# Performance work log

Measured on AMD Instinct MI355X. Metric: run time of the kernel, lower is better.

The kernel has to match this reference:

```python
import jax, jax.numpy as jnp
import numpy as np

B, T, A, OBS = 4096, 32, 4, 115
H, K, ACT = 64, 8, 19
FEAT = 4 + 3 + 4 * A          # 23 structured features
IN_DIM = FEAT + ACT * A       # 99 with action one-hots


def setup_inputs() -> dict:
    key = jax.random.key(0)
    ks = jax.random.split(key, 16)
    s = lambda *sh: 1.0 / np.sqrt(sh[-1])
    inp = {
        "obs_seq": jax.random.normal(ks[0], (B, T, A, OBS), jnp.float32),
        "action_seq": jax.random.randint(ks[1], (B, T, A), 0, ACT, jnp.int32),
        # feature_proj: Linear(IN_DIM->H) + LayerNorm(H)
        "proj_W": jax.random.normal(ks[2], (H, IN_DIM), jnp.float32) * s(H, IN_DIM),
        "proj_b": jnp.zeros((H,), jnp.float32),
        "ln_g": jnp.ones((H,), jnp.float32),
        "ln_b": jnp.zeros((H,), jnp.float32),
        # 2-layer GRU
        "Wih0": jax.random.normal(ks[3], (3 * H, H), jnp.float32) * s(1, H),
        "Whh0": jax.random.normal(ks[4], (3 * H, H), jnp.float32) * s(1, H),
        "bih0": jnp.zeros((3 * H,), jnp.float32),
        "bhh0": jnp.zeros((3 * H,), jnp.float32),
        "Wih1": jax.random.normal(ks[5], (3 * H, H), jnp.float32) * s(1, H),
        "Whh1": jax.random.normal(ks[6], (3 * H, H), jnp.float32) * s(1, H),
        "bih1": jnp.zeros((3 * H,), jnp.float32),
        "bhh1": jnp.zeros((3 * H,), jnp.float32),
        # classifier MLP
        "cls_W1": jax.random.normal(ks[7], (H, H), jnp.float32) * s(H, H),
        "cls_b1": jnp.zeros((H,), jnp.float32),
        "cls_W2": jax.random.normal(ks[8], (K, H), jnp.float32) * s(K, H),
        "cls_b2": jnp.zeros((K,), jnp.float32),
    }
    return inp


def _extract_features(obs_seq, action_seq):
    b, t, a = obs_seq.shape[:3]
    # ball position from player 0's obs, and its finite-difference velocity
    ball_pos = obs_seq[:, :, 0, 88:90]                       # [B,T,2]
    ball_vel = jnp.concatenate(
        [jnp.zeros_like(ball_pos[:, :1]), ball_pos[:, 1:] - ball_pos[:, :-1]], axis=1)
    pos = obs_seq[..., 0:2]                                   # [B,T,A,2]
    pos_flat = pos.reshape(b, t, a * 2)
    centroid = pos.mean(axis=2)                               # [B,T,2]
    spread = jnp.sqrt(((pos - centroid[:, :, None]) ** 2).sum(-1).mean(2, keepdims=True) + 1e-6)
    # closest-teammate relative position: vectorized argmin over pairwise dists
    diff = pos[:, :, :, None, :] - pos[:, :, None, :, :]      # [B,T,A,A,2]
    d2 = (diff ** 2).sum(-1)                                  # [B,T,A,A]
    d2 = jnp.where(jnp.eye(a, dtype=bool), jnp.inf, d2)       # exclude self
    idx = jnp.argmin(d2, axis=-1)                             # [B,T,A]
    nearest = jnp.take_along_axis(pos, idx[..., None], axis=2)  # [B,T,A,2]
    closest_rel = (nearest - pos).reshape(b, t, a * 2)
    onehot = jax.nn.one_hot(action_seq, ACT, dtype=jnp.float32).reshape(b, t, a * ACT)
    return jnp.concatenate(
        [ball_pos, ball_vel, pos_flat, centroid, spread, closest_rel, onehot], axis=-1)


def _gru_layer(x_tbh, Wih, Whh, bih, bhh):
    h0 = jnp.zeros((x_tbh.shape[1], Whh.shape[1]), x_tbh.dtype)

    def step(h, x):
        gi = x @ Wih.T + bih
        gh = h @ Whh.T + bhh
        ir, iz, inn = jnp.split(gi, 3, axis=-1)
        hr, hz, hn = jnp.split(gh, 3, axis=-1)
        r = jax.nn.sigmoid(ir + hr)
        z = jax.nn.sigmoid(iz + hz)
        n = jnp.tanh(inn + r * hn)
        h_new = (1.0 - z) * n + z * h
        return h_new, h_new

    h_last, ys = jax.lax.scan(step, h0, x_tbh)
    return ys, h_last


def reference(obs_seq, action_seq, proj_W, proj_b, ln_g, ln_b,
              Wih0, Whh0, bih0, bhh0, Wih1, Whh1, bih1, bhh1,
              cls_W1, cls_b1, cls_W2, cls_b2):
    feats = _extract_features(obs_seq, action_seq)            # [B,T,99]
    x = feats @ proj_W.T + proj_b                             # [B,T,H]
    mu = x.mean(-1, keepdims=True)
    var = x.var(-1, keepdims=True)
    x = (x - mu) * jax.lax.rsqrt(var + 1e-5) * ln_g + ln_b
    x = jax.nn.relu(x)
    x = jnp.swapaxes(x, 0, 1)                                 # [T,B,H]
    ys0, _ = _gru_layer(x, Wih0, Whh0, bih0, bhh0)
    _, h_last = _gru_layer(ys0, Wih1, Whh1, bih1, bhh1)       # [B,H]
    hid = jax.nn.relu(h_last @ cls_W1.T + cls_b1)
    logits = hid @ cls_W2.T + cls_b2                          # [B,K]
    return logits
```

## Files before the change

### kernel.cpp

```cpp
#include <hip/hip_runtime.h>

#define B_ 4096
#define T_ 32
#define A_ 4
#define OBS_ 115
#define H_ 64
#define IN_DIM_ 99
#define ACT_ 19
#define NBT (B_*T_)

typedef _Float16 f16;
typedef _Float16 f16x8 __attribute__((ext_vector_type(8)));
typedef float f32x4 __attribute__((ext_vector_type(4)));

static __device__ __forceinline__ float sigmoid_f(float x) {
    return __builtin_amdgcn_rcpf(1.f + __expf(-x));
}
static __device__ __forceinline__ float tanh_f(float x) {
    return 1.f - 2.f * __builtin_amdgcn_rcpf(1.f + __expf(2.f * x));
}
static __device__ __forceinline__ f32x4 mfma16(f16x8 a, f16x8 b, f32x4 c) {
    return __builtin_amdgcn_mfma_f32_16x16x32_f16(a, b, c, 0, 0, 0);
}

__global__ __launch_bounds__(256) void k0_transpose(const float* __restrict__ W,
                                                    float* __restrict__ WT) {
    int idx = blockIdx.x * 256 + threadIdx.x;
    if (idx < IN_DIM_ * H_) {
        int i = idx >> 6, h = idx & 63;
        WT[idx] = W[h * IN_DIM_ + i];
    }
}

__global__ __launch_bounds__(256) void k1_fused(const float* __restrict__ obs,
                                                const int* __restrict__ act,
                                                const float* __restrict__ WT,
                                                const float* __restrict__ pb,
                                                const float* __restrict__ lng,
                                                const float* __restrict__ lnb,
                                                f16* __restrict__ xout) {
    __shared__ float fl[256 * 25];
    __shared__ int al[256 * 5];
    int tid = threadIdx.x;
    int n = blockIdx.x * 256 + tid;
    const float* o = obs + (size_t)n * (A_ * OBS_);

    float px[A_], py[A_];
#pragma unroll
    for (int a = 0; a < A_; a++) { px[a] = o[a * OBS_]; py[a] = o[a * OBS_ + 1]; }
    float bx = o[88], by = o[89];
    int t0 = n & (T_ - 1);
    float pbx = bx, pby = by;
    if (t0 > 0) { pbx = o[88 - A_ * OBS_]; pby = o[89 - A_ * OBS_]; }

    float cx = (px[0] + px[1] + px[2] + px[3]) * 0.25f;
    float cy = (py[0] + py[1] + py[2] + py[3]) * 0.25f;
    float sp = 0.f;
#pragma unroll
    for (int a = 0; a < A_; a++) { float dx = px[a] - cx, dy = py[a] - cy; sp += dx * dx + dy * dy; }
    sp = sqrtf(sp * 0.25f + 1e-6f);

    float crx[A_], cry[A_];
#pragma unroll
    for (int i = 0; i < A_; i++) {
        float best = 3.4e38f; int bj = 0;
#pragma unroll
        for (int j = 0; j < A_; j++) {
            if (j == i) continue;
            float dx = px[i] - px[j], dy = py[i] - py[j];
            float d2 = dx * dx + dy * dy;
            if (d2 < best) { best = d2; bj = j; }
        }
        crx[i] = px[bj] - px[i]; cry[i] = py[bj] - py[i];
    }

    float* f = &fl[tid * 25];
    f[0] = bx; f[1] = by; f[2] = bx - pbx; f[3] = by - pby;
#pragma unroll
    for (int a = 0; a < A_; a++) { f[4 + 2 * a] = px[a]; f[5 + 2 * a] = py[a]; }
    f[12] = cx; f[13] = cy; f[14] = sp;
#pragma unroll
    for (int a = 0; a < A_; a++) { f[15 + 2 * a] = crx[a]; f[16 + 2 * a] = cry[a]; }
#pragma unroll
    for (int a = 0; a < A_; a++) al[tid * 5 + a] = act[n * A_ + a];
    __syncthreads();

    int lane = tid & 63;
    int wv = __builtin_amdgcn_readfirstlane(tid >> 6);
    float wc[23];
#pragma unroll
    for (int i = 0; i < 23; i++) wc[i] = WT[i * 64 + lane];
    float pbv = pb[lane], g = lng[lane], bb = lnb[lane];
    int b0 = blockIdx.x * 8 + wv * 2;

    for (int it = 0; it < 64; it++) {
        int lb = wv * 64 + it;
        int b = b0 + (it >> 5);
        int t = it & 31;
        const float* fp = &fl[lb * 25];
        float v = pbv;
#pragma unroll
        for (int i = 0; i < 23; i++) v += fp[i] * wc[i];
#pragma unroll
        for (int a = 0; a < A_; a++) {
            int ai = al[lb * 5 + a];
            v += WT[(23 + a * ACT_ + ai) * 64 + lane];
        }
        float s = v, ss = v * v;
#pragma unroll
        for (int m = 1; m < 64; m <<= 1) {
            s += __shfl_xor(s, m, 64);
            ss += __shfl_xor(ss, m, 64);
        }
        float mean = s * (1.f / 64.f);
        float var = ss * (1.f / 64.f) - mean * mean;
        float xn = (v - mean) * rsqrtf(var + 1e-5f) * g + bb;
        xn = fmaxf(xn, 0.f);
        xout[((size_t)t * B_ + b) * 64 + lane] = (f16)xn;
    }
}

__global__ __launch_bounds__(512, 1) void k2_gru(
        const f16* __restrict__ x,
        const float* __restrict__ Wih0, const float* __restrict__ Whh0,
        const float* __restrict__ bih0, const float* __restrict__ bhh0,
        const float* __restrict__ Wih1, const float* __restrict__ Whh1,
        const float* __restrict__ bih1, const float* __restrict__ bhh1,
        const float* __restrict__ W1, const float* __restrict__ b1,
        const float* __restrict__ W2, const float* __restrict__ b2,
        float* __restrict__ out) {
    __shared__ __align__(16) f16 hbuf[2][2][16 * 72];
    int tid = threadIdx.x;
    int lane = tid & 63;
    int wv = __builtin_amdgcn_readfirstlane(tid >> 6);
    int L = wv >> 2;
    int S = (wv & 3) * 16;
    int c = lane & 15, q = lane >> 4;
    int rowbase = blockIdx.x * 16;

    for (int k = tid; k < 2 * 2 * 16 * 72; k += 512) ((f16*)hbuf)[k] = (f16)0.f;

    auto ldw = [&](const float* W, int row0, int kcol) -> f16x8 {
        const float* p = W + (size_t)(row0 + c) * 64 + kcol + q * 8;
        f32x4 w0 = *(const f32x4*)p;
        f32x4 w1 = *(const f32x4*)(p + 4);
        f16x8 r;
        r[0] = (f16)w0[0]; r[1] = (f16)w0[1]; r[2] = (f16)w0[2]; r[3] = (f16)w0[3];
        r[4] = (f16)w1[0]; r[5] = (f16)w1[1]; r[6] = (f16)w1[2]; r[7] = (f16)w1[3];
        return r;
    };

    const float* Wih = L ? Wih1 : Wih0;
    const float* Whh = L ? Whh1 : Whh0;
    const float* bih = L ? bih1 : bih0;
    const float* bhh = L ? bhh1 : bhh0;

    f16x8 wih[3][2], whh[3][2];
#pragma unroll
    for (int g = 0; g < 3; g++)
#pragma unroll
        for (int kf = 0; kf < 2; kf++) {
            wih[g][kf] = ldw(Wih, g * 64 + S, kf * 32);
            whh[g][kf] = ldw(Whh, g * 64 + S, kf * 32);
        }

    float br = bih[S + c] + bhh[S + c];
    float bz = bih[64 + S + c] + bhh[64 + S + c];
    float bi = bih[128 + S + c];
    float bh = bhh[128 + S + c];
    f32x4 vbr = {br, br, br, br}, vbz = {bz, bz, bz, bz};
    f32x4 vbi = {bi, bi, bi, bi}, vbh = {bh, bh, bh, bh};

    f32x4 hc = {0.f, 0.f, 0.f, 0.f};

    auto ldx = [&](int t, int kf) -> f16x8 {
        return *(const f16x8*)(x + ((size_t)t * B_ + rowbase + c) * 64 + kf * 32 + q * 8);
    };

    __syncthreads();

    int p = 0;
    f16x8 xa0 = {}, xa1 = {}, xn0 = {}, xn1 = {};
    if (L == 0) { xa0 = ldx(0, 0); xa1 = ldx(0, 1); xn0 = xa0; xn1 = xa1; }

    for (int i = 0; i <= T_; i++) {
        f16x8 hh0, hh1, in0, in1;
        if (L == 0) {
            if (i + 1 < T_) { xn0 = ldx(i + 1, 0); xn1 = ldx(i + 1, 1); }
            hh0 = *(const f16x8*)&hbuf[0][p][c * 72 + q * 8];
            hh1 = *(const f16x8*)&hbuf[0][p][c * 72 + 32 + q * 8];
            in0 = xa0; in1 = xa1;
        } else {
            hh0 = *(const f16x8*)&hbuf[1][p][c * 72 + q * 8];
            hh1 = *(const f16x8*)&hbuf[1][p][c * 72 + 32 + q * 8];
            in0 = *(const f16x8*)&hbuf[0][p][c * 72 + q * 8];
            in1 = *(const f16x8*)&hbuf[0][p][c * 72 + 32 + q * 8];
        }
        bool active = L ? (i > 0) : (i < T_);
        if (active) {
            f32x4 r = vbr, z = vbz, in_ = vbi, hn = vbh;
            r = mfma16(hh0, whh[0][0], r); r = mfma16(hh1, whh[0][1], r);
            r = mfma16(in0, wih[0][0], r); r = mfma16(in1, wih[0][1], r);
            z = mfma16(hh0, whh[1][0], z); z = mfma16(hh1, whh[1][1], z);
            z = mfma16(in0, wih[1][0], z); z = mfma16(in1, wih[1][1], z);
            in_ = mfma16(in0, wih[2][0], in_); in_ = mfma16(in1, wih[2][1], in_);
            hn = mfma16(hh0, whh[2][0], hn); hn = mfma16(hh1, whh[2][1], hn);
#pragma unroll
            for (int rr = 0; rr < 4; rr++) {
                float rg = sigmoid_f(r[rr]);
                float zg = sigmoid_f(z[rr]);
                float ng = tanh_f(in_[rr] + rg * hn[rr]);
                hc[rr] = ng + zg * (hc[rr] - ng);
            }
        }
#pragma unroll
        for (int rr = 0; rr < 4; rr++)
            hbuf[L][p ^ 1][(q * 4 + rr) * 72 + S + c] = (f16)hc[rr];
        __syncthreads();
        p ^= 1;
        if (L == 0) { xa0 = xn0; xa1 = xn1; }
    }

    f16x8 ha0 = *(const f16x8*)&hbuf[1][p][c * 72 + q * 8];
    f16x8 ha1 = *(const f16x8*)&hbuf[1][p][c * 72 + 32 + q * 8];
    if (L == 0) {
        f16x8 w1f0 = ldw(W1, S, 0), w1f1 = ldw(W1, S, 32);
        float bw1 = b1[S + c];
        f32x4 hid = {bw1, bw1, bw1, bw1};
        hid = mfma16(ha0, w1f0, hid);
        hid = mfma16(ha1, w1f1, hid);
#pragma unroll
        for (int rr = 0; rr < 4; rr++) {
            float hv = fmaxf(hid[rr], 0.f);
            hbuf[0][p ^ 1][(q * 4 + rr) * 72 + S + c] = (f16)hv;
        }
    }
    __syncthreads();
    if (wv == 0) {
        f16x8 ga0 = *(const f16x8*)&hbuf[0][p ^ 1][c * 72 + q * 8];
        f16x8 ga1 = *(const f16x8*)&hbuf[0][p ^ 1][c * 72 + 32 + q * 8];
        f16x8 w2f0 = {}, w2f1 = {};
        float bo = 0.f;
        if (c < 8) {
            w2f0 = ldw(W2, 0, 0);
            w2f1 = ldw(W2, 0, 32);
            bo = b2[c];
        }
        f32x4 lg = {bo, bo, bo, bo};
        lg = mfma16(ga0, w2f0, lg);
        lg = mfma16(ga1, w2f1, lg);
        if (c < 8) {
#pragma unroll
            for (int rr = 0; rr < 4; rr++)
                out[(size_t)(rowbase + q * 4 + rr) * 8 + c] = lg[rr];
        }
    }
}

extern "C" void kernel_launch(void* const* d_in, const int* in_sizes, int n_in,
                              void* d_out, int out_size, void* d_ws, size_t ws_size,
                              hipStream_t stream) {
    const float* obs  = (const float*)d_in[0];
    const int*   act  = (const int*)d_in[1];
    const float* projW = (const float*)d_in[2];
    const float* projb = (const float*)d_in[3];
    const float* lng  = (const float*)d_in[4];
    const float* lnb  = (const float*)d_in[5];
    const float* Wih0 = (const float*)d_in[6];
    const float* Whh0 = (const float*)d_in[7];
    const float* bih0 = (const float*)d_in[8];
    const float* bhh0 = (const float*)d_in[9];
    const float* Wih1 = (const float*)d_in[10];
    const float* Whh1 = (const float*)d_in[11];
    const float* bih1 = (const float*)d_in[12];
    const float* bhh1 = (const float*)d_in[13];
    const float* W1   = (const float*)d_in[14];
    const float* b1   = (const float*)d_in[15];
    const float* W2   = (const float*)d_in[16];
    const float* b2   = (const float*)d_in[17];
    float* out = (float*)d_out;

    char* ws = (char*)d_ws;
    float* WT = (float*)ws;
    f16*   xw = (f16*)(ws + 32768);

    k0_transpose<<<25, 256, 0, stream>>>(projW, WT);
    k1_fused<<<NBT / 256, 256, 0, stream>>>(obs, act, WT, projb, lng, lnb, xw);
    k2_gru<<<B_ / 16, 512, 0, stream>>>(xw, Wih0, Whh0, bih0, bhh0,
                                        Wih1, Whh1, bih1, bhh1,
                                        W1, b1, W2, b2, out);
}
```

Before: 394.9 us.

## Fuse feature extraction, projection and GRU into a single kernel via LDS

Merges the weight transpose, feature/projection/LayerNorm kernel and GRU kernel into one launch. Each block computes features for its 16 sequences, stages the transposed projection weight and normalized inputs in shared memory, then runs the GRU reading inputs from LDS instead of global memory. This removes the intermediate global write/read of the activations and extra launches, but uses ~157KB LDS per block and loses the overlap between independent feature blocks and the GRU; each block also redundantly transposes projW. Action indices are packed into bytes.

```diff
diff --git a/kernel.cpp b/kernel.cpp
--- a/kernel.cpp
+++ b/kernel.cpp
@@ -23,105 +23,10 @@
     return __builtin_amdgcn_mfma_f32_16x16x32_f16(a, b, c, 0, 0, 0);
 }
 
-__global__ __launch_bounds__(256) void k0_transpose(const float* __restrict__ W,
-                                                    float* __restrict__ WT) {
-    int idx = blockIdx.x * 256 + threadIdx.x;
-    if (idx < IN_DIM_ * H_) {
-        int i = idx >> 6, h = idx & 63;
-        WT[idx] = W[h * IN_DIM_ + i];
-    }
-}
-
-__global__ __launch_bounds__(256) void k1_fused(const float* __restrict__ obs,
-                                                const int* __restrict__ act,
-                                                const float* __restrict__ WT,
-                                                const float* __restrict__ pb,
-                                                const float* __restrict__ lng,
-                                                const float* __restrict__ lnb,
-                                                f16* __restrict__ xout) {
-    __shared__ float fl[256 * 25];
-    __shared__ int al[256 * 5];
-    int tid = threadIdx.x;
-    int n = blockIdx.x * 256 + tid;
-    const float* o = obs + (size_t)n * (A_ * OBS_);
-
-    float px[A_], py[A_];
-#pragma unroll
-    for (int a = 0; a < A_; a++) { px[a] = o[a * OBS_]; py[a] = o[a * OBS_ + 1]; }
-    float bx = o[88], by = o[89];
-    int t0 = n & (T_ - 1);
-    float pbx = bx, pby = by;
-    if (t0 > 0) { pbx = o[88 - A_ * OBS_]; pby = o[89 - A_ * OBS_]; }
-
-    float cx = (px[0] + px[1] + px[2] + px[3]) * 0.25f;
-    float cy = (py[0] + py[1] + py[2] + py[3]) * 0.25f;
-    float sp = 0.f;
-#pragma unroll
-    for (int a = 0; a < A_; a++) { float dx = px[a] - cx, dy = py[a] - cy; sp += dx * dx + dy * dy; }
-    sp = sqrtf(sp * 0.25f + 1e-6f);
-
-    float crx[A_], cry[A_];
-#pragma unroll
-    for (int i = 0; i < A_; i++) {
-        float best = 3.4e38f; int bj = 0;
-#pragma unroll
-        for (int j = 0; j < A_; j++) {
-            if (j == i) continue;
-            float dx = px[i] - px[j], dy = py[i] - py[j];
-            float d2 = dx * dx + dy * dy;
-            if (d2 < best) { best = d2; bj = j; }
-        }
-        crx[i] = px[bj] - px[i]; cry[i] = py[bj] - py[i];
-    }
-
-    float* f = &fl[tid * 25];
-    f[0] = bx; f[1] = by; f[2] = bx - pbx; f[3] = by - pby;
-#pragma unroll
-    for (int a = 0; a < A_; a++) { f[4 + 2 * a] = px[a]; f[5 + 2 * a] = py[a]; }
-    f[12] = cx; f[13] = cy; f[14] = sp;
-#pragma unroll
-    for (int a = 0; a < A_; a++) { f[15 + 2 * a] = crx[a]; f[16 + 2 * a] = cry[a]; }
-#pragma unroll
-    for (int a = 0; a < A_; a++) al[tid * 5 + a] = act[n * A_ + a];
-    __syncthreads();
-
-    int lane = tid & 63;
-    int wv = __builtin_amdgcn_readfirstlane(tid >> 6);
-    float wc[23];
-#pragma unroll
-    for (int i = 0; i < 23; i++) wc[i] = WT[i * 64 + lane];
-    float pbv = pb[lane], g = lng[lane], bb = lnb[lane];
-    int b0 = blockIdx.x * 8 + wv * 2;
-
-    for (int it = 0; it < 64; it++) {
-        int lb = wv * 64 + it;
-        int b = b0 + (it >> 5);
-        int t = it & 31;
-        const float* fp = &fl[lb * 25];
-        float v = pbv;
-#pragma unroll
-        for (int i = 0; i < 23; i++) v += fp[i] * wc[i];
-#pragma unroll
-        for (int a = 0; a < A_; a++) {
-            int ai = al[lb * 5 + a];
-            v += WT[(23 + a * ACT_ + ai) * 64 + lane];
-        }
-        float s = v, ss = v * v;
-#pragma unroll
-        for (int m = 1; m < 64; m <<= 1) {
-            s += __shfl_xor(s, m, 64);
-            ss += __shfl_xor(ss, m, 64);
-        }
-        float mean = s * (1.f / 64.f);
-        float var = ss * (1.f / 64.f) - mean * mean;
-        float xn = (v - mean) * rsqrtf(var + 1e-5f) * g + bb;
-        xn = fmaxf(xn, 0.f);
-        xout[((size_t)t * B_ + b) * 64 + lane] = (f16)xn;
-    }
-}
-
-__global__ __launch_bounds__(512, 1) void k2_gru(
-        const f16* __restrict__ x,
+__global__ __launch_bounds__(512, 1) void fused_all(
+        const float* __restrict__ obs, const int* __restrict__ act,
+        const float* __restrict__ projW, const float* __restrict__ pb,
+        const float* __restrict__ lng, const float* __restrict__ lnb,
         const float* __restrict__ Wih0, const float* __restrict__ Whh0,
         const float* __restrict__ bih0, const float* __restrict__ bhh0,
         const float* __restrict__ Wih1, const float* __restrict__ Whh1,
@@ -129,16 +34,17 @@
         const float* __restrict__ W1, const float* __restrict__ b1,
         const float* __restrict__ W2, const float* __restrict__ b2,
         float* __restrict__ out) {
+    __shared__ float fl[512 * 25];
+    __shared__ float wtl[IN_DIM_ * 64];
+    __shared__ int al[512];
+    __shared__ __align__(16) f16 xls[32 * 16 * 72];
     __shared__ __align__(16) f16 hbuf[2][2][16 * 72];
+
     int tid = threadIdx.x;
     int lane = tid & 63;
     int wv = __builtin_amdgcn_readfirstlane(tid >> 6);
-    int L = wv >> 2;
-    int S = (wv & 3) * 16;
     int c = lane & 15, q = lane >> 4;
     int rowbase = blockIdx.x * 16;
-
-    for (int k = tid; k < 2 * 2 * 16 * 72; k += 512) ((f16*)hbuf)[k] = (f16)0.f;
 
     auto ldw = [&](const float* W, int row0, int kcol) -> f16x8 {
         const float* p = W + (size_t)(row0 + c) * 64 + kcol + q * 8;
@@ -149,12 +55,12 @@
         r[4] = (f16)w1[0]; r[5] = (f16)w1[1]; r[6] = (f16)w1[2]; r[7] = (f16)w1[3];
         return r;
     };
-
+    int L = wv >> 2;
+    int S = (wv & 3) * 16;
     const float* Wih = L ? Wih1 : Wih0;
     const float* Whh = L ? Whh1 : Whh0;
     const float* bih = L ? bih1 : bih0;
     const float* bhh = L ? bhh1 : bhh0;
-
     f16x8 wih[3][2], whh[3][2];
 #pragma unroll
     for (int g = 0; g < 3; g++)
@@ -163,7 +69,6 @@
             wih[g][kf] = ldw(Wih, g * 64 + S, kf * 32);
             whh[g][kf] = ldw(Whh, g * 64 + S, kf * 32);
         }
-
     float br = bih[S + c] + bhh[S + c];
     float bz = bih[64 + S + c] + bhh[64 + S + c];
     float bi = bih[128 + S + c];
@@ -171,25 +76,106 @@
     f32x4 vbr = {br, br, br, br}, vbz = {bz, bz, bz, bz};
     f32x4 vbi = {bi, bi, bi, bi}, vbh = {bh, bh, bh, bh};
 
+    {
+        int n = blockIdx.x * 512 + tid;
+        const float* o = obs + (size_t)n * (A_ * OBS_);
+        float px[A_], py[A_];
+#pragma unroll
+        for (int a = 0; a < A_; a++) {
+            float2 p2 = *(const float2*)&o[a * OBS_];
+            px[a] = p2.x; py[a] = p2.y;
+        }
+        float2 bl = *(const float2*)&o[88];
+        int t0 = tid & 31;
+        float2 pbl = bl;
+        if (t0 > 0) pbl = *(const float2*)&o[88 - A_ * OBS_];
+
+        float cx = (px[0] + px[1] + px[2] + px[3]) * 0.25f;
+        float cy = (py[0] + py[1] + py[2] + py[3]) * 0.25f;
+        float sp = 0.f;
+#pragma unroll
+        for (int a = 0; a < A_; a++) { float dx = px[a] - cx, dy = py[a] - cy; sp += dx * dx + dy * dy; }
+        sp = sqrtf(sp * 0.25f + 1e-6f);
+
+        float crx[A_], cry[A_];
+#pragma unroll
+        for (int i = 0; i < A_; i++) {
+            float best = 3.4e38f; int bj = 0;
+#pragma unroll
+            for (int j = 0; j < A_; j++) {
+                if (j == i) continue;
+                float dx = px[i] - px[j], dy = py[i] - py[j];
+                float d2 = dx * dx + dy * dy;
+                if (d2 < best) { best = d2; bj = j; }
+            }
+            crx[i] = px[bj] - px[i]; cry[i] = py[bj] - py[i];
+        }
+
+        float* f = &fl[tid * 25];
+        f[0] = bl.x; f[1] = bl.y; f[2] = bl.x - pbl.x; f[3] = bl.y - pbl.y;
+#pragma unroll
+        for (int a = 0; a < A_; a++) { f[4 + 2 * a] = px[a]; f[5 + 2 * a] = py[a]; }
+        f[12] = cx; f[13] = cy; f[14] = sp;
+#pragma unroll
+        for (int a = 0; a < A_; a++) { f[15 + 2 * a] = crx[a]; f[16 + 2 * a] = cry[a]; }
+
+        int4 av = *(const int4*)&act[n * A_];
+        al[tid] = av.x | (av.y << 8) | (av.z << 16) | (av.w << 24);
+
+        for (int k = tid; k < IN_DIM_ * 64; k += 512) {
+            int h = k / 64, i = k & 63;
+            int hh = k / IN_DIM_, ii = k - hh * IN_DIM_;
+            (void)h; (void)i;
+            wtl[ii * 64 + hh] = projW[k];
+        }
+        for (int k = tid; k < 2 * 2 * 16 * 72; k += 512) ((f16*)hbuf)[k] = (f16)0.f;
+    }
+    __syncthreads();
+
+    {
+        float wc[23];
+#pragma unroll
+        for (int i = 0; i < 23; i++) wc[i] = wtl[i * 64 + lane];
+        float pbv = pb[lane], g = lng[lane], bb = lnb[lane];
+
+        for (int it = 0; it < 64; it++) {
+            int lb = wv * 64 + it;
+            int r = lb >> 5, t = lb & 31;
+            const float* fp = &fl[lb * 25];
+            float v = pbv;
+#pragma unroll
+            for (int i = 0; i < 23; i++) v += fp[i] * wc[i];
+            int a4 = al[lb];
+#pragma unroll
+            for (int a = 0; a < A_; a++) {
+                int ai = (a4 >> (8 * a)) & 0xFF;
+                v += wtl[(23 + a * ACT_ + ai) * 64 + lane];
+            }
+            float s = v, ss = v * v;
+#pragma unroll
+            for (int m = 1; m < 64; m <<= 1) {
+                s += __shfl_xor(s, m, 64);
+                ss += __shfl_xor(ss, m, 64);
+            }
+            float mean = s * (1.f / 64.f);
+            float var = ss * (1.f / 64.f) - mean * mean;
+            float xn = (v - mean) * rsqrtf(var + 1e-5f) * g + bb;
+            xn = fmaxf(xn, 0.f);
+            xls[(t * 16 + r) * 72 + lane] = (f16)xn;
+        }
+    }
+    __syncthreads();
+
     f32x4 hc = {0.f, 0.f, 0.f, 0.f};
-
-    auto ldx = [&](int t, int kf) -> f16x8 {
-        return *(const f16x8*)(x + ((size_t)t * B_ + rowbase + c) * 64 + kf * 32 + q * 8);
-    };
-
-    __syncthreads();
-
     int p = 0;
-    f16x8 xa0 = {}, xa1 = {}, xn0 = {}, xn1 = {};
-    if (L == 0) { xa0 = ldx(0, 0); xa1 = ldx(0, 1); xn0 = xa0; xn1 = xa1; }
-
     for (int i = 0; i <= T_; i++) {
         f16x8 hh0, hh1, in0, in1;
         if (L == 0) {
-            if (i + 1 < T_) { xn0 = ldx(i + 1, 0); xn1 = ldx(i + 1, 1); }
             hh0 = *(const f16x8*)&hbuf[0][p][c * 72 + q * 8];
             hh1 = *(const f16x8*)&hbuf[0][p][c * 72 + 32 + q * 8];
-            in0 = xa0; in1 = xa1;
+            int t = (i < T_) ? i : (T_ - 1);
+            in0 = *(const f16x8*)&xls[(t * 16 + c) * 72 + q * 8];
+            in1 = *(const f16x8*)&xls[(t * 16 + c) * 72 + 32 + q * 8];
         } else {
             hh0 = *(const f16x8*)&hbuf[1][p][c * 72 + q * 8];
             hh1 = *(const f16x8*)&hbuf[1][p][c * 72 + 32 + q * 8];
@@ -218,7 +204,6 @@
             hbuf[L][p ^ 1][(q * 4 + rr) * 72 + S + c] = (f16)hc[rr];
         __syncthreads();
         p ^= 1;
-        if (L == 0) { xa0 = xn0; xa1 = xn1; }
     }
 
     f16x8 ha0 = *(const f16x8*)&hbuf[1][p][c * 72 + q * 8];
@@ -280,13 +265,8 @@
     const float* b2   = (const float*)d_in[17];
     float* out = (float*)d_out;
 
-    char* ws = (char*)d_ws;
-    float* WT = (float*)ws;
-    f16*   xw = (f16*)(ws + 32768);
-
-    k0_transpose<<<25, 256, 0, stream>>>(projW, WT);
-    k1_fused<<<NBT / 256, 256, 0, stream>>>(obs, act, WT, projb, lng, lnb, xw);
-    k2_gru<<<B_ / 16, 512, 0, stream>>>(xw, Wih0, Whh0, bih0, bhh0,
-                                        Wih1, Whh1, bih1, bhh1,
-                                        W1, b1, W2, b2, out);
-}
+    fused_all<<<B_ / 16, 512, 0, stream>>>(obs, act, projW, projb, lng, lnb,
+                                           Wih0, Whh0, bih0, bhh0,
+                                           Wih1, Whh1, bih1, bhh1,
+                                           W1, b1, W2, b2, out);
+}
```

Measured after the change: 386.0 us. 1.02x faster.
